# Kernel optimization log

Hardware: AMD Instinct MI355X
Metric: run time of the kernel (lower is better)

## Reference

```python
import jax, jax.numpy as jnp
import numpy as np

B, S, D = 8, 1024, 1024
H, DH = 16, 64
FF = 4096
EPS = 1e-5


def setup_inputs() -> dict:
    key = jax.random.key(0)
    ks = jax.random.split(key, 16)
    sd = 1.0 / np.sqrt(D)
    sp = 1.0 / np.sqrt(H * DH)
    sf = 1.0 / np.sqrt(FF)
    return {
        "x": jax.random.normal(ks[0], (B, S, D), jnp.float32),
        # per-head QKV projections stacked: [H, D, DH]
        "wq": jax.random.uniform(ks[1], (H, D, DH), jnp.float32, -sd, sd),
        "bq": jax.random.uniform(ks[2], (H, DH), jnp.float32, -sd, sd),
        "wk": jax.random.uniform(ks[3], (H, D, DH), jnp.float32, -sd, sd),
        "bk": jax.random.uniform(ks[4], (H, DH), jnp.float32, -sd, sd),
        "wv": jax.random.uniform(ks[5], (H, D, DH), jnp.float32, -sd, sd),
        "bv": jax.random.uniform(ks[6], (H, DH), jnp.float32, -sd, sd),
        "wo": jax.random.uniform(ks[7], (H * DH, D), jnp.float32, -sp, sp),
        "bo": jax.random.uniform(ks[8], (D,), jnp.float32, -sp, sp),
        "w1": jax.random.uniform(ks[9], (D, FF), jnp.float32, -sd, sd),
        "b1": jax.random.uniform(ks[10], (FF,), jnp.float32, -sd, sd),
        "w2": jax.random.uniform(ks[11], (FF, D), jnp.float32, -sf, sf),
        "b2": jax.random.uniform(ks[12], (D,), jnp.float32, -sf, sf),
        "g1": jnp.ones((D,), jnp.float32),
        "be1": jnp.zeros((D,), jnp.float32),
        "g2": jnp.ones((D,), jnp.float32),
        "be2": jnp.zeros((D,), jnp.float32),
    }


def _layernorm(x, g, b):
    mu = jnp.mean(x, axis=-1, keepdims=True)
    var = jnp.mean((x - mu) ** 2, axis=-1, keepdims=True)
    return (x - mu) * jax.lax.rsqrt(var + EPS) * g + b


def reference(x, wq, bq, wk, bk, wv, bv, wo, bo, w1, b1, w2, b2, g1, be1, g2, be2):
    # batched multi-head attention (math identical to the per-head torch loop)
    q = jnp.einsum('bsd,hde->bhse', x, wq) + bq[None, :, None, :]
    k = jnp.einsum('bsd,hde->bhse', x, wk) + bk[None, :, None, :]
    v = jnp.einsum('bsd,hde->bhse', x, wv) + bv[None, :, None, :]
    scores = jnp.einsum('bhse,bhte->bhst', q, k) / jnp.sqrt(jnp.float32(DH))
    probs = jax.nn.softmax(scores, axis=-1)
    ctx = jnp.einsum('bhst,bhte->bhse', probs, v)  # [B,H,S,DH]
    ctx = ctx.transpose(0, 2, 1, 3).reshape(B, S, H * DH)  # concat over heads
    attn = ctx @ wo + bo
    # dropout is identity in eval mode
    x = _layernorm(x + attn, g1, be1)
    ffn = jax.nn.relu(x @ w1 + b1) @ w2 + b2
    x = _layernorm(x + ffn, g2, be2)
    return x
```

## Files before the change

### kernel.cpp

```cpp
#include <hip/hip_runtime.h>
#include <hip/hip_bf16.h>

#define Bb 8
#define Ss 1024
#define Dd 1024
#define Hh 16
#define DHh 64
#define FFf 4096

typedef __hip_bfloat16 bf16;
typedef __attribute__((ext_vector_type(8))) __bf16 bf16x8;
typedef __attribute__((ext_vector_type(4))) float f32x4;

__device__ __forceinline__ unsigned short f2bu(float f) {
  __hip_bfloat16 h = __float2bfloat16(f);
  return __builtin_bit_cast(unsigned short, h);
}

#define MFMA16(a, b, c) __builtin_amdgcn_mfma_f32_16x16x32_bf16((a), (b), (c), 0, 0, 0)

__device__ __forceinline__ void gl_lds16(const void* g, void* l) {
  __builtin_amdgcn_global_load_lds(
      (const __attribute__((address_space(1))) unsigned int*)g,
      (__attribute__((address_space(3))) unsigned int*)l, 16, 0, 0);
}

__global__ __launch_bounds__(256) void f32_to_bf16_vec(const float* __restrict__ in,
                                                       bf16* __restrict__ out, int n4) {
  int i = blockIdx.x * 256 + threadIdx.x;
  if (i < n4) {
    float4 v = ((const float4*)in)[i];
    union { unsigned short u[4]; uint2 q; } r;
    r.u[0] = f2bu(v.x); r.u[1] = f2bu(v.y); r.u[2] = f2bu(v.z); r.u[3] = f2bu(v.w);
    ((uint2*)out)[i] = r.q;
  }
}

__global__ __launch_bounds__(256) void transpose_f32_bf16(const float* __restrict__ src,
                                                          bf16* __restrict__ dst,
                                                          int R, int C,
                                                          long sbatch, long dbatch) {
  __shared__ float tile[32][33];
  src += (size_t)blockIdx.z * sbatch;
  dst += (size_t)blockIdx.z * dbatch;
  int c0 = blockIdx.x * 32, r0 = blockIdx.y * 32;
  int tx = threadIdx.x & 31;
  int ty = threadIdx.x >> 5;
#pragma unroll
  for (int kk = 0; kk < 4; ++kk)
    tile[ty + kk * 8][tx] = src[(size_t)(r0 + ty + kk * 8) * C + c0 + tx];
  __syncthreads();
#pragma unroll
  for (int kk = 0; kk < 4; ++kk)
    dst[(size_t)(c0 + ty + kk * 8) * R + r0 + tx] = __float2bfloat16(tile[tx][ty + kk * 8]);
}

enum { EPI_QKV = 0, EPI_WO = 1, EPI_FFN1 = 2, EPI_FFN2 = 3 };

template <int EPI>
__global__ __launch_bounds__(256) void gemm_bt(const bf16* __restrict__ A,
                                               const bf16* __restrict__ Bt,
                                               int M, int N, int K,
                                               const float* __restrict__ bias0,
                                               const float* __restrict__ bias1,
                                               const float* __restrict__ bias2,
                                               void* __restrict__ o0,
                                               void* __restrict__ o1,
                                               void* __restrict__ o2) {
  __shared__ __align__(16) unsigned char sm[16384];
  const int t = threadIdx.x;
  const int lane = t & 63;
  const int w = t >> 6;
  const int wr = w >> 1;
  const int wc = w & 1;
  const int m0 = blockIdx.x * 128;
  const int n0 = blockIdx.y * 128;

  f32x4 acc[4][4];
  const f32x4 z4 = {0.f, 0.f, 0.f, 0.f};
#pragma unroll
  for (int i = 0; i < 4; ++i)
#pragma unroll
    for (int j = 0; j < 4; ++j) acc[i][j] = z4;

  const int srow = lane >> 2;
  const int sseg = lane & 3;
  const int ks = lane >> 4;
  const int rl = lane & 15;

  for (int kt = 0; kt < K; kt += 32) {
    __syncthreads();
#pragma unroll
    for (int r = 0; r < 2; ++r) {
      const int arow = r * 64 + w * 16 + srow;
      const int aseg = sseg ^ (arow & 3);
      gl_lds16(A + ((size_t)(m0 + arow) * K + kt + aseg * 8),
               sm + r * 4096 + w * 1024);
      const int brow = r * 64 + w * 16 + srow;
      const int bseg = sseg ^ (brow & 3);
      gl_lds16(Bt + ((size_t)(n0 + brow) * K + kt + bseg * 8),
               sm + 8192 + r * 4096 + w * 1024);
    }
    __syncthreads();
    bf16x8 a[4], b[4];
#pragma unroll
    for (int i = 0; i < 4; ++i) {
      const int row = wr * 64 + i * 16 + rl;
      a[i] = *(const bf16x8*)(sm + row * 64 + (ks ^ (row & 3)) * 16);
      const int col = wc * 64 + i * 16 + rl;
      b[i] = *(const bf16x8*)(sm + 8192 + col * 64 + (ks ^ (col & 3)) * 16);
    }
#pragma unroll
    for (int i = 0; i < 4; ++i)
#pragma unroll
      for (int j = 0; j < 4; ++j) acc[i][j] = MFMA16(a[i], b[j], acc[i][j]);
  }

  const int rbase = (lane >> 4) * 4;
  if constexpr (EPI == EPI_QKV) {
    const int which = n0 >> 10;
    const float* bias = which == 0 ? bias0 : (which == 1 ? bias1 : bias2);
    bf16* dst = (bf16*)(which == 0 ? o0 : (which == 1 ? o1 : o2));
#pragma unroll
    for (int i = 0; i < 4; ++i) {
#pragma unroll
      for (int j = 0; j < 4; ++j) {
        const int gcol = n0 + wc * 64 + j * 16 + rl;
        const int cc = gcol & 1023;
        const int hh = cc >> 6, e = cc & 63;
        const float bval = bias[cc];
#pragma unroll
        for (int p = 0; p < 4; ++p) {
          const int grow = m0 + wr * 64 + i * 16 + rbase + p;
          const int bidx = grow >> 10, s = grow & 1023;
          if (which == 2) {
            dst[(((size_t)bidx * Hh + hh) * DHh + e) * Ss + s] =
                __float2bfloat16(acc[i][j][p] + bval);
          } else {
            dst[(((size_t)bidx * Hh + hh) * Ss + s) * DHh + e] =
                __float2bfloat16(acc[i][j][p] + bval);
          }
        }
      }
    }
  } else if constexpr (EPI == EPI_WO || EPI == EPI_FFN2) {
    float* dst = (float*)o0;
#pragma unroll
    for (int i = 0; i < 4; ++i) {
#pragma unroll
      for (int j = 0; j < 4; ++j) {
        const int gcol = n0 + wc * 64 + j * 16 + rl;
        const float bval = bias0[gcol];
#pragma unroll
        for (int p = 0; p < 4; ++p) {
          const int grow = m0 + wr * 64 + i * 16 + rbase + p;
          dst[(size_t)grow * N + gcol] = acc[i][j][p] + bval;
        }
      }
    }
  } else {
    bf16* dst = (bf16*)o0;
#pragma unroll
    for (int i = 0; i < 4; ++i) {
#pragma unroll
      for (int j = 0; j < 4; ++j) {
        const int gcol = n0 + wc * 64 + j * 16 + rl;
        const float bval = bias0[gcol];
#pragma unroll
        for (int p = 0; p < 4; ++p) {
          const int grow = m0 + wr * 64 + i * 16 + rbase + p;
          dst[(size_t)grow * N + gcol] =
              __float2bfloat16(fmaxf(acc[i][j][p] + bval, 0.f));
        }
      }
    }
  }
}

__global__ __launch_bounds__(256) void attn_kernel(const bf16* __restrict__ q,
                                                   const bf16* __restrict__ k,
                                                   const bf16* __restrict__ v,
                                                   bf16* __restrict__ ctx) {
  __shared__ __align__(16) unsigned short Kl[64 * 64];
  __shared__ __align__(16) unsigned short Vt[64 * 64];
  __shared__ __align__(16) unsigned short Pl[4 * 16 * 72];

  const int bid = blockIdx.x;
  const int xcd = bid & 7;
  const int s8 = bid >> 3;
  const int hg = xcd + 8 * (s8 >> 4);
  const int qi = s8 & 15;
  const int b = hg >> 4, h = hg & 15;
  const int q0 = qi * 64;
  const size_t head = (size_t)hg << 16;
  const bf16* Qp = q + head;
  const bf16* Kp = k + head;
  const bf16* Vp = v + head;

  const int t = threadIdx.x;
  const int w = t >> 6;
  const int lane = t & 63;
  const int rl = lane & 15;
  const int ks = lane >> 4;
  const int rx = rl & 7;

  const int qrow = q0 + w * 16 + rl;
  const bf16x8 aq0 = *(const bf16x8*)(Qp + (size_t)qrow * 64 + ks * 8);
  const bf16x8 aq1 = *(const bf16x8*)(Qp + (size_t)qrow * 64 + 32 + ks * 8);

  f32x4 o[4];
  const f32x4 z4 = {0.f, 0.f, 0.f, 0.f};
#pragma unroll
  for (int c = 0; c < 4; ++c) o[c] = z4;
  float m4[4] = {-1e30f, -1e30f, -1e30f, -1e30f};
  float l4[4] = {0.f, 0.f, 0.f, 0.f};

  const int srow8 = lane >> 3;
  const int sseg = lane & 7;
  unsigned short* Pw = Pl + w * 16 * 72;
  const float scale = 0.125f;

  for (int kv0 = 0; kv0 < Ss; kv0 += 64) {
    __syncthreads();
#pragma unroll
    for (int r = 0; r < 2; ++r) {
      const int rb = w * 16 + r * 8;
      const int row = rb + srow8;
      gl_lds16(Kp + (size_t)(kv0 + row) * 64 + (sseg ^ (row & 7)) * 8,
               Kl + rb * 64);
      gl_lds16(Vp + (size_t)row * Ss + kv0 + (sseg ^ (row & 7)) * 8,
               Vt + rb * 64);
    }
    __syncthreads();

    f32x4 s4[4];
#pragma unroll
    for (int f = 0; f < 4; ++f) s4[f] = z4;
#pragma unroll
    for (int f = 0; f < 4; ++f) {
      const int row = f * 16 + rl;
      const bf16x8 b0 = *(const bf16x8*)(Kl + row * 64 + (ks ^ rx) * 8);
      const bf16x8 b1 = *(const bf16x8*)(Kl + row * 64 + ((4 + ks) ^ rx) * 8);
      s4[f] = MFMA16(aq0, b0, s4[f]);
      s4[f] = MFMA16(aq1, b1, s4[f]);
    }

    float mx[4], sm[4];
#pragma unroll
    for (int j = 0; j < 4; ++j) {
      s4[0][j] *= scale; s4[1][j] *= scale; s4[2][j] *= scale; s4[3][j] *= scale;
      mx[j] = fmaxf(fmaxf(s4[0][j], s4[1][j]), fmaxf(s4[2][j], s4[3][j]));
    }
#pragma unroll
    for (int mm = 1; mm < 16; mm <<= 1)
#pragma unroll
      for (int j = 0; j < 4; ++j) mx[j] = fmaxf(mx[j], __shfl_xor(mx[j], mm, 64));
#pragma unroll
    for (int j = 0; j < 4; ++j) {
      const float mn = fmaxf(m4[j], mx[j]);
      const float corr = __expf(m4[j] - mn);
      m4[j] = mn;
#pragma unroll
      for (int f = 0; f < 4; ++f) s4[f][j] = __expf(s4[f][j] - mn);
      sm[j] = (s4[0][j] + s4[1][j]) + (s4[2][j] + s4[3][j]);
      l4[j] *= corr;
#pragma unroll
      for (int c = 0; c < 4; ++c) o[c][j] *= corr;
    }
#pragma unroll
    for (int mm = 1; mm < 16; mm <<= 1)
#pragma unroll
      for (int j = 0; j < 4; ++j) sm[j] += __shfl_xor(sm[j], mm, 64);
#pragma unroll
    for (int j = 0; j < 4; ++j) l4[j] += sm[j];

#pragma unroll
    for (int f = 0; f < 4; ++f)
#pragma unroll
      for (int j = 0; j < 4; ++j)
        Pw[(ks * 4 + j) * 72 + f * 16 + rl] = f2bu(s4[f][j]);
    asm volatile("s_waitcnt lgkmcnt(0)" ::: "memory");
    __builtin_amdgcn_sched_barrier(0);
    const bf16x8 pa0 = *(const bf16x8*)(Pw + rl * 72 + ks * 8);
    const bf16x8 pa1 = *(const bf16x8*)(Pw + rl * 72 + 32 + ks * 8);

#pragma unroll
    for (int c = 0; c < 4; ++c) {
      const int row = c * 16 + rl;
      const bf16x8 v0 = *(const bf16x8*)(Vt + row * 64 + (ks ^ rx) * 8);
      const bf16x8 v1 = *(const bf16x8*)(Vt + row * 64 + ((4 + ks) ^ rx) * 8);
      o[c] = MFMA16(pa0, v0, o[c]);
      o[c] = MFMA16(pa1, v1, o[c]);
    }
  }

  float inv[4];
#pragma unroll
  for (int j = 0; j < 4; ++j) inv[j] = 1.0f / l4[j];
#pragma unroll
  for (int c = 0; c < 4; ++c) {
#pragma unroll
    for (int j = 0; j < 4; ++j) {
      const int sq = q0 + w * 16 + ks * 4 + j;
      const int dh = c * 16 + rl;
      ctx[(((size_t)b * Ss + sq) * Hh + h) * DHh + dh] =
          __float2bfloat16(o[c][j] * inv[j]);
    }
  }
}

__global__ __launch_bounds__(256) void ln_fused(const float* __restrict__ a,
                                                const float* __restrict__ bsrc,
                                                const float* __restrict__ g,
                                                const float* __restrict__ be,
                                                float* __restrict__ of,
                                                bf16* __restrict__ ob) {
  const int row = blockIdx.x, t = threadIdx.x;
  const float4 va = ((const float4*)(a + (size_t)row * Dd))[t];
  const float4 vb = ((const float4*)(bsrc + (size_t)row * Dd))[t];
  const float x0 = va.x + vb.x, x1 = va.y + vb.y, x2 = va.z + vb.z, x3 = va.w + vb.w;
  float s = x0 + x1 + x2 + x3;
  float qq = x0 * x0 + x1 * x1 + x2 * x2 + x3 * x3;
#pragma unroll
  for (int m = 1; m < 64; m <<= 1) {
    s += __shfl_xor(s, m, 64);
    qq += __shfl_xor(qq, m, 64);
  }
  __shared__ float ss[4], sq2[4];
  if ((t & 63) == 0) {
    ss[t >> 6] = s;
    sq2[t >> 6] = qq;
  }
  __syncthreads();
  s = ss[0] + ss[1] + ss[2] + ss[3];
  qq = sq2[0] + sq2[1] + sq2[2] + sq2[3];
  const float mu = s * (1.0f / Dd);
  const float var = qq * (1.0f / Dd) - mu * mu;
  const float rs = rsqrtf(var + 1e-5f);
  const float4 gv = ((const float4*)g)[t];
  const float4 bv = ((const float4*)be)[t];
  const float y0 = (x0 - mu) * rs * gv.x + bv.x;
  const float y1 = (x1 - mu) * rs * gv.y + bv.y;
  const float y2 = (x2 - mu) * rs * gv.z + bv.z;
  const float y3 = (x3 - mu) * rs * gv.w + bv.w;
  if (of) ((float4*)(of + (size_t)row * Dd))[t] = make_float4(y0, y1, y2, y3);
  if (ob) {
    union { unsigned short u[4]; uint2 qv; } r;
    r.u[0] = f2bu(y0); r.u[1] = f2bu(y1); r.u[2] = f2bu(y2); r.u[3] = f2bu(y3);
    ((uint2*)(ob + (size_t)row * Dd))[t] = r.qv;
  }
}

extern "C" void kernel_launch(void* const* d_in, const int* in_sizes, int n_in,
                              void* d_out, int out_size, void* d_ws, size_t ws_size,
                              hipStream_t stream) {
  const float* x   = (const float*)d_in[0];
  const float* wq  = (const float*)d_in[1];
  const float* bq  = (const float*)d_in[2];
  const float* wk  = (const float*)d_in[3];
  const float* bk  = (const float*)d_in[4];
  const float* wv  = (const float*)d_in[5];
  const float* bv  = (const float*)d_in[6];
  const float* wo  = (const float*)d_in[7];
  const float* bo  = (const float*)d_in[8];
  const float* w1  = (const float*)d_in[9];
  const float* b1  = (const float*)d_in[10];
  const float* w2  = (const float*)d_in[11];
  const float* b2  = (const float*)d_in[12];
  const float* g1  = (const float*)d_in[13];
  const float* be1 = (const float*)d_in[14];
  const float* g2  = (const float*)d_in[15];
  const float* be2 = (const float*)d_in[16];
  float* out = (float*)d_out;

  char* ws = (char*)d_ws;
  const size_t MB = 1u << 20;
  bf16* qb    = (bf16*)(ws + 0);
  bf16* kb    = (bf16*)(ws + 16 * MB);
  bf16* vvb   = (bf16*)(ws + 32 * MB);
  bf16* xb    = (bf16*)(ws + 48 * MB);
  bf16* hb    = (bf16*)(ws + 0);
  bf16* ctx   = (bf16*)(ws + 64 * MB);
  float* y    = (float*)(ws + 80 * MB);
  float* x1f  = (float*)(ws + 112 * MB);
  bf16* x1b   = (bf16*)(ws + 144 * MB);
  bf16* btqkv = (bf16*)(ws + 160 * MB);
  bf16* wot   = (bf16*)(ws + 166 * MB);
  bf16* w1t   = (bf16*)(ws + 168 * MB);
  bf16* w2t   = (bf16*)(ws + 176 * MB);

  f32_to_bf16_vec<<<8192, 256, 0, stream>>>(x, xb, Bb * Ss * Dd / 4);
  transpose_f32_bf16<<<dim3(2, 32, 16), 256, 0, stream>>>(wq, btqkv + 0 * 1048576,
                                                          Dd, DHh, 65536, 65536);
  transpose_f32_bf16<<<dim3(2, 32, 16), 256, 0, stream>>>(wk, btqkv + 1 * 1048576,
                                                          Dd, DHh, 65536, 65536);
  transpose_f32_bf16<<<dim3(2, 32, 16), 256, 0, stream>>>(wv, btqkv + 2 * 1048576,
                                                          Dd, DHh, 65536, 65536);
  transpose_f32_bf16<<<dim3(32, 32, 1), 256, 0, stream>>>(wo, wot, Hh * DHh, Dd, 0, 0);
  transpose_f32_bf16<<<dim3(128, 32, 1), 256, 0, stream>>>(w1, w1t, Dd, FFf, 0, 0);
  transpose_f32_bf16<<<dim3(32, 128, 1), 256, 0, stream>>>(w2, w2t, FFf, Dd, 0, 0);

  gemm_bt<EPI_QKV><<<dim3(64, 24), 256, 0, stream>>>(
      xb, btqkv, Bb * Ss, 3 * Hh * DHh, Dd, bq, bk, bv, qb, kb, vvb);

  attn_kernel<<<2048, 256, 0, stream>>>(qb, kb, vvb, ctx);

  gemm_bt<EPI_WO><<<dim3(64, 8), 256, 0, stream>>>(
      ctx, wot, Bb * Ss, Dd, Hh * DHh, bo, nullptr, nullptr, y, nullptr, nullptr);

  ln_fused<<<Bb * Ss, 256, 0, stream>>>(x, y, g1, be1, x1f, x1b);

  gemm_bt<EPI_FFN1><<<dim3(64, 32), 256, 0, stream>>>(
      x1b, w1t, Bb * Ss, FFf, Dd, b1, nullptr, nullptr, hb, nullptr, nullptr);
  gemm_bt<EPI_FFN2><<<dim3(64, 8), 256, 0, stream>>>(
      hb, w2t, Bb * Ss, Dd, FFf, b2, nullptr, nullptr, y, nullptr, nullptr);

  ln_fused<<<Bb * Ss, 256, 0, stream>>>(x1f, y, g2, be2, out, nullptr);
}
```

Measured before the change: 596.4 us.

## Replace 128x128 GEMM with double-buffered 256x256 tiled GEMM using staged prefetch

Replaces the 128x128-tile, K=32 single-buffered GEMM with a 256x256-tile, K=64 kernel using 512 threads, 128KB of dynamic LDS and double buffering. Loads for the next A tile and the tile after next for B are issued in between MFMA quarter-steps, with barriers, setprio and manual vmcnt waits, so global loads overlap compute. An XCD-aware block swizzle is added. The larger tiles reduce global traffic per FLOP but lower the block count: WO and FFN2 run only 128 blocks on a 256-CU device, which risks under-occupancy. The 128KB LDS request also limits residency per CU.

```diff
diff --git a/kernel.cpp b/kernel.cpp
--- a/kernel.cpp
+++ b/kernel.cpp
@@ -57,88 +57,163 @@
 
 enum { EPI_QKV = 0, EPI_WO = 1, EPI_FFN1 = 2, EPI_FFN2 = 3 };
 
+__device__ __forceinline__ void stage_tile(const bf16* __restrict__ G, int ldK,
+                                           int row0, int t, int u,
+                                           unsigned char* ldsbase, int tid) {
+  const int r = u * 64 + (tid >> 3);
+  const int seg = (tid & 7) ^ (((tid >> 3) & 1) << 2);
+  gl_lds16(G + (size_t)(row0 + r) * ldK + t * 64 + seg * 8,
+           ldsbase + u * 8192 + (tid >> 6) * 1024);
+}
+
 template <int EPI>
-__global__ __launch_bounds__(256) void gemm_bt(const bf16* __restrict__ A,
-                                               const bf16* __restrict__ Bt,
-                                               int M, int N, int K,
-                                               const float* __restrict__ bias0,
-                                               const float* __restrict__ bias1,
-                                               const float* __restrict__ bias2,
-                                               void* __restrict__ o0,
-                                               void* __restrict__ o1,
-                                               void* __restrict__ o2) {
-  __shared__ __align__(16) unsigned char sm[16384];
-  const int t = threadIdx.x;
-  const int lane = t & 63;
-  const int w = t >> 6;
-  const int wr = w >> 1;
-  const int wc = w & 1;
-  const int m0 = blockIdx.x * 128;
-  const int n0 = blockIdx.y * 128;
-
-  f32x4 acc[4][4];
+__global__ __launch_bounds__(512, 2) void gemm256(const bf16* __restrict__ A,
+                                                  const bf16* __restrict__ Bt,
+                                                  int M, int N, int K,
+                                                  const float* __restrict__ bias0,
+                                                  const float* __restrict__ bias1,
+                                                  const float* __restrict__ bias2,
+                                                  void* __restrict__ o0,
+                                                  void* __restrict__ o1,
+                                                  void* __restrict__ o2) {
+  extern __shared__ __align__(16) unsigned char sm[];
+  const int tid = threadIdx.x;
+  const int lane = tid & 63;
+  const int w = tid >> 6;
+  const int wr = w >> 2, wc = w & 3;
+  const int rl = lane & 15, ks4 = lane >> 4;
+  const int NTm = M >> 8, NTn = N >> 8;
+  const int nwg = NTm * NTn;
+  const int swz = (blockIdx.x & 7) * (nwg >> 3) + (blockIdx.x >> 3);
+  const int mt = swz % NTm, nt = swz / NTm;
+  const int m0 = mt << 8, n0 = nt << 8;
+  const int NT = K >> 6;
+
+  f32x4 acc[8][4];
   const f32x4 z4 = {0.f, 0.f, 0.f, 0.f};
 #pragma unroll
-  for (int i = 0; i < 4; ++i)
+  for (int i = 0; i < 8; ++i)
 #pragma unroll
     for (int j = 0; j < 4; ++j) acc[i][j] = z4;
 
-  const int srow = lane >> 2;
-  const int sseg = lane & 3;
-  const int ks = lane >> 4;
-  const int rl = lane & 15;
-
-  for (int kt = 0; kt < K; kt += 32) {
-    __syncthreads();
-#pragma unroll
-    for (int r = 0; r < 2; ++r) {
-      const int arow = r * 64 + w * 16 + srow;
-      const int aseg = sseg ^ (arow & 3);
-      gl_lds16(A + ((size_t)(m0 + arow) * K + kt + aseg * 8),
-               sm + r * 4096 + w * 1024);
-      const int brow = r * 64 + w * 16 + srow;
-      const int bseg = sseg ^ (brow & 3);
-      gl_lds16(Bt + ((size_t)(n0 + brow) * K + kt + bseg * 8),
-               sm + 8192 + r * 4096 + w * 1024);
-    }
-    __syncthreads();
-    bf16x8 a[4], b[4];
-#pragma unroll
-    for (int i = 0; i < 4; ++i) {
-      const int row = wr * 64 + i * 16 + rl;
-      a[i] = *(const bf16x8*)(sm + row * 64 + (ks ^ (row & 3)) * 16);
-      const int col = wc * 64 + i * 16 + rl;
-      b[i] = *(const bf16x8*)(sm + 8192 + col * 64 + (ks ^ (col & 3)) * 16);
-    }
-#pragma unroll
-    for (int i = 0; i < 4; ++i)
-#pragma unroll
-      for (int j = 0; j < 4; ++j) acc[i][j] = MFMA16(a[i], b[j], acc[i][j]);
-  }
-
-  const int rbase = (lane >> 4) * 4;
+#pragma unroll
+  for (int u = 0; u < 4; ++u) stage_tile(A, K, m0, 0, u, sm, tid);
+#pragma unroll
+  for (int u = 0; u < 4; ++u) stage_tile(Bt, K, n0, 0, u, sm + 32768, tid);
+  if (NT > 1) {
+#pragma unroll
+    for (int u = 0; u < 4; ++u) stage_tile(Bt, K, n0, 1, u, sm + 65536 + 32768, tid);
+    asm volatile("s_waitcnt vmcnt(4)" ::: "memory");
+  } else {
+    asm volatile("s_waitcnt vmcnt(0)" ::: "memory");
+  }
+  __builtin_amdgcn_s_barrier();
+
+  for (int t = 0; t < NT; ++t) {
+    unsigned char* Al = sm + ((t & 1) << 16);
+    unsigned char* Bl = Al + 32768;
+    unsigned char* AlN = sm + (((t + 1) & 1) << 16);
+    bf16x8 bfr[4][2], afr[2][2];
+
+#pragma unroll
+    for (int fc = 0; fc < 4; ++fc)
+#pragma unroll
+      for (int kk = 0; kk < 2; ++kk) {
+        const int rr = wc * 64 + fc * 16 + rl;
+        bfr[fc][kk] = *(const bf16x8*)(Bl + rr * 128 + ((kk ^ (rr & 1)) << 6) + ks4 * 16);
+      }
+#pragma unroll
+    for (int i = 0; i < 2; ++i)
+#pragma unroll
+      for (int kk = 0; kk < 2; ++kk) {
+        const int r = wr * 128 + i * 16 + rl;
+        afr[i][kk] = *(const bf16x8*)(Al + r * 128 + ((kk ^ (r & 1)) << 6) + ks4 * 16);
+      }
+    if (t + 1 < NT) {
+      stage_tile(A, K, m0, t + 1, 0, AlN, tid);
+      stage_tile(A, K, m0, t + 1, 2, AlN, tid);
+    }
+    __builtin_amdgcn_s_barrier();
+    __builtin_amdgcn_s_setprio(1);
+#pragma unroll
+    for (int i = 0; i < 2; ++i)
+#pragma unroll
+      for (int fc = 0; fc < 4; ++fc)
+#pragma unroll
+        for (int kk = 0; kk < 2; ++kk)
+          acc[i][fc] = MFMA16(afr[i][kk], bfr[fc][kk], acc[i][fc]);
+    __builtin_amdgcn_s_setprio(0);
+    __builtin_amdgcn_s_barrier();
+
+#pragma unroll
+    for (int q = 1; q < 4; ++q) {
+#pragma unroll
+      for (int i = 0; i < 2; ++i)
+#pragma unroll
+        for (int kk = 0; kk < 2; ++kk) {
+          const int r = wr * 128 + (q * 2 + i) * 16 + rl;
+          afr[i][kk] = *(const bf16x8*)(Al + r * 128 + ((kk ^ (r & 1)) << 6) + ks4 * 16);
+        }
+      if (q == 1) {
+        if (t + 1 < NT) {
+          stage_tile(A, K, m0, t + 1, 1, AlN, tid);
+          stage_tile(A, K, m0, t + 1, 3, AlN, tid);
+        }
+      } else if (q == 2) {
+        if (t + 2 < NT) {
+          stage_tile(Bt, K, n0, t + 2, 0, Bl, tid);
+          stage_tile(Bt, K, n0, t + 2, 1, Bl, tid);
+        }
+      } else {
+        if (t + 2 < NT) {
+          stage_tile(Bt, K, n0, t + 2, 2, Bl, tid);
+          stage_tile(Bt, K, n0, t + 2, 3, Bl, tid);
+        }
+      }
+      __builtin_amdgcn_s_barrier();
+      __builtin_amdgcn_s_setprio(1);
+#pragma unroll
+      for (int i = 0; i < 2; ++i)
+#pragma unroll
+        for (int fc = 0; fc < 4; ++fc)
+#pragma unroll
+          for (int kk = 0; kk < 2; ++kk)
+            acc[q * 2 + i][fc] = MFMA16(afr[i][kk], bfr[fc][kk], acc[q * 2 + i][fc]);
+      __builtin_amdgcn_s_setprio(0);
+      if (q == 3) {
+        if (t + 2 < NT) {
+          asm volatile("s_waitcnt vmcnt(4)" ::: "memory");
+        } else if (t + 1 < NT) {
+          asm volatile("s_waitcnt vmcnt(0)" ::: "memory");
+        }
+      }
+      __builtin_amdgcn_s_barrier();
+    }
+  }
+
+  const int rbase = ks4 * 4;
   if constexpr (EPI == EPI_QKV) {
     const int which = n0 >> 10;
     const float* bias = which == 0 ? bias0 : (which == 1 ? bias1 : bias2);
     bf16* dst = (bf16*)(which == 0 ? o0 : (which == 1 ? o1 : o2));
 #pragma unroll
-    for (int i = 0; i < 4; ++i) {
-#pragma unroll
-      for (int j = 0; j < 4; ++j) {
-        const int gcol = n0 + wc * 64 + j * 16 + rl;
+    for (int fr = 0; fr < 8; ++fr) {
+#pragma unroll
+      for (int fc = 0; fc < 4; ++fc) {
+        const int gcol = n0 + wc * 64 + fc * 16 + rl;
         const int cc = gcol & 1023;
         const int hh = cc >> 6, e = cc & 63;
         const float bval = bias[cc];
 #pragma unroll
         for (int p = 0; p < 4; ++p) {
-          const int grow = m0 + wr * 64 + i * 16 + rbase + p;
+          const int grow = m0 + wr * 128 + fr * 16 + rbase + p;
           const int bidx = grow >> 10, s = grow & 1023;
           if (which == 2) {
             dst[(((size_t)bidx * Hh + hh) * DHh + e) * Ss + s] =
-                __float2bfloat16(acc[i][j][p] + bval);
+                __float2bfloat16(acc[fr][fc][p] + bval);
           } else {
             dst[(((size_t)bidx * Hh + hh) * Ss + s) * DHh + e] =
-                __float2bfloat16(acc[i][j][p] + bval);
+                __float2bfloat16(acc[fr][fc][p] + bval);
           }
         }
       }
@@ -146,31 +221,31 @@
   } else if constexpr (EPI == EPI_WO || EPI == EPI_FFN2) {
     float* dst = (float*)o0;
 #pragma unroll
-    for (int i = 0; i < 4; ++i) {
-#pragma unroll
-      for (int j = 0; j < 4; ++j) {
-        const int gcol = n0 + wc * 64 + j * 16 + rl;
+    for (int fr = 0; fr < 8; ++fr) {
+#pragma unroll
+      for (int fc = 0; fc < 4; ++fc) {
+        const int gcol = n0 + wc * 64 + fc * 16 + rl;
         const float bval = bias0[gcol];
 #pragma unroll
         for (int p = 0; p < 4; ++p) {
-          const int grow = m0 + wr * 64 + i * 16 + rbase + p;
-          dst[(size_t)grow * N + gcol] = acc[i][j][p] + bval;
+          const int grow = m0 + wr * 128 + fr * 16 + rbase + p;
+          dst[(size_t)grow * N + gcol] = acc[fr][fc][p] + bval;
         }
       }
     }
   } else {
     bf16* dst = (bf16*)o0;
 #pragma unroll
-    for (int i = 0; i < 4; ++i) {
-#pragma unroll
-      for (int j = 0; j < 4; ++j) {
-        const int gcol = n0 + wc * 64 + j * 16 + rl;
+    for (int fr = 0; fr < 8; ++fr) {
+#pragma unroll
+      for (int fc = 0; fc < 4; ++fc) {
+        const int gcol = n0 + wc * 64 + fc * 16 + rl;
         const float bval = bias0[gcol];
 #pragma unroll
         for (int p = 0; p < 4; ++p) {
-          const int grow = m0 + wr * 64 + i * 16 + rbase + p;
+          const int grow = m0 + wr * 128 + fr * 16 + rbase + p;
           dst[(size_t)grow * N + gcol] =
-              __float2bfloat16(fmaxf(acc[i][j][p] + bval, 0.f));
+              __float2bfloat16(fmaxf(acc[fr][fc][p] + bval, 0.f));
         }
       }
     }
@@ -400,19 +475,19 @@
   transpose_f32_bf16<<<dim3(128, 32, 1), 256, 0, stream>>>(w1, w1t, Dd, FFf, 0, 0);
   transpose_f32_bf16<<<dim3(32, 128, 1), 256, 0, stream>>>(w2, w2t, FFf, Dd, 0, 0);
 
-  gemm_bt<EPI_QKV><<<dim3(64, 24), 256, 0, stream>>>(
+  gemm256<EPI_QKV><<<384, 512, 131072, stream>>>(
       xb, btqkv, Bb * Ss, 3 * Hh * DHh, Dd, bq, bk, bv, qb, kb, vvb);
 
   attn_kernel<<<2048, 256, 0, stream>>>(qb, kb, vvb, ctx);
 
-  gemm_bt<EPI_WO><<<dim3(64, 8), 256, 0, stream>>>(
+  gemm256<EPI_WO><<<128, 512, 131072, stream>>>(
       ctx, wot, Bb * Ss, Dd, Hh * DHh, bo, nullptr, nullptr, y, nullptr, nullptr);
 
   ln_fused<<<Bb * Ss, 256, 0, stream>>>(x, y, g1, be1, x1f, x1b);
 
-  gemm_bt<EPI_FFN1><<<dim3(64, 32), 256, 0, stream>>>(
+  gemm256<EPI_FFN1><<<512, 512, 131072, stream>>>(
       x1b, w1t, Bb * Ss, FFf, Dd, b1, nullptr, nullptr, hb, nullptr, nullptr);
-  gemm_bt<EPI_FFN2><<<dim3(64, 8), 256, 0, stream>>>(
+  gemm256<EPI_FFN2><<<128, 512, 131072, stream>>>(
       hb, w2t, Bb * Ss, Dd, FFf, b2, nullptr, nullptr, y, nullptr, nullptr);
 
   ln_fused<<<Bb * Ss, 256, 0, stream>>>(x1f, y, g2, be2, out, nullptr);
```

Result: slower. 700.3 us (+17.4%).

## Double GEMM k-tile depth and register-prefetch next K/V tile in attention

Applied to the files above, without the earlier changes.

The GEMM kernel now stages 64-wide K tiles (32 KB LDS) with an 8-way XOR swizzle, doing two MFMAs per fragment pair per barrier pair. This halves the number of sync rounds per output tile. The attention kernel replaces direct global-to-LDS loads with register prefetch of the next K/V tile, issued after the current tile is written to LDS, so the global loads overlap with compute. The cost is higher LDS use, which may lower occupancy, and extra VGPRs for the prefetch registers.

```diff
diff --git a/kernel.cpp b/kernel.cpp
--- a/kernel.cpp
+++ b/kernel.cpp
@@ -57,6 +57,15 @@
 
 enum { EPI_QKV = 0, EPI_WO = 1, EPI_FFN1 = 2, EPI_FFN2 = 3 };
 
+__device__ __forceinline__ void stage_u(const bf16* __restrict__ G, int ldK,
+                                        int row0, int kt, int u,
+                                        unsigned char* ldsbase, int tid) {
+  const int r = u * 32 + (tid >> 3);
+  const int seg = (tid & 7) ^ (r & 7);
+  gl_lds16(G + (size_t)(row0 + r) * ldK + kt + seg * 8,
+           ldsbase + u * 4096 + (tid >> 6) * 1024);
+}
+
 template <int EPI>
 __global__ __launch_bounds__(256) void gemm_bt(const bf16* __restrict__ A,
                                                const bf16* __restrict__ Bt,
@@ -67,7 +76,7 @@
                                                void* __restrict__ o0,
                                                void* __restrict__ o1,
                                                void* __restrict__ o2) {
-  __shared__ __align__(16) unsigned char sm[16384];
+  __shared__ __align__(16) unsigned char sm[32768];
   const int t = threadIdx.x;
   const int lane = t & 63;
   const int w = t >> 6;
@@ -75,6 +84,7 @@
   const int wc = w & 1;
   const int m0 = blockIdx.x * 128;
   const int n0 = blockIdx.y * 128;
+  const int rl = lane & 15, ks = lane >> 4;
 
   f32x4 acc[4][4];
   const f32x4 z4 = {0.f, 0.f, 0.f, 0.f};
@@ -83,40 +93,35 @@
 #pragma unroll
     for (int j = 0; j < 4; ++j) acc[i][j] = z4;
 
-  const int srow = lane >> 2;
-  const int sseg = lane & 3;
-  const int ks = lane >> 4;
-  const int rl = lane & 15;
-
-  for (int kt = 0; kt < K; kt += 32) {
+  for (int kt = 0; kt < K; kt += 64) {
     __syncthreads();
 #pragma unroll
-    for (int r = 0; r < 2; ++r) {
-      const int arow = r * 64 + w * 16 + srow;
-      const int aseg = sseg ^ (arow & 3);
-      gl_lds16(A + ((size_t)(m0 + arow) * K + kt + aseg * 8),
-               sm + r * 4096 + w * 1024);
-      const int brow = r * 64 + w * 16 + srow;
-      const int bseg = sseg ^ (brow & 3);
-      gl_lds16(Bt + ((size_t)(n0 + brow) * K + kt + bseg * 8),
-               sm + 8192 + r * 4096 + w * 1024);
-    }
+    for (int u = 0; u < 4; ++u) stage_u(A, K, m0, kt, u, sm, t);
+#pragma unroll
+    for (int u = 0; u < 4; ++u) stage_u(Bt, K, n0, kt, u, sm + 16384, t);
     __syncthreads();
-    bf16x8 a[4], b[4];
+
+    bf16x8 a[4][2], b[4][2];
 #pragma unroll
     for (int i = 0; i < 4; ++i) {
-      const int row = wr * 64 + i * 16 + rl;
-      a[i] = *(const bf16x8*)(sm + row * 64 + (ks ^ (row & 3)) * 16);
-      const int col = wc * 64 + i * 16 + rl;
-      b[i] = *(const bf16x8*)(sm + 8192 + col * 64 + (ks ^ (col & 3)) * 16);
+#pragma unroll
+      for (int kk = 0; kk < 2; ++kk) {
+        const int row = wr * 64 + i * 16 + rl;
+        a[i][kk] = *(const bf16x8*)(sm + row * 128 + (((kk * 4 + ks) ^ (row & 7)) << 4));
+        const int col = wc * 64 + i * 16 + rl;
+        b[i][kk] = *(const bf16x8*)(sm + 16384 + col * 128 + (((kk * 4 + ks) ^ (col & 7)) << 4));
+      }
     }
 #pragma unroll
     for (int i = 0; i < 4; ++i)
 #pragma unroll
-      for (int j = 0; j < 4; ++j) acc[i][j] = MFMA16(a[i], b[j], acc[i][j]);
-  }
-
-  const int rbase = (lane >> 4) * 4;
+      for (int j = 0; j < 4; ++j)
+#pragma unroll
+        for (int kk = 0; kk < 2; ++kk)
+          acc[i][j] = MFMA16(a[i][kk], b[j][kk], acc[i][j]);
+  }
+
+  const int rbase = ks * 4;
   if constexpr (EPI == EPI_QKV) {
     const int which = n0 >> 10;
     const float* bias = which == 0 ? bias0 : (which == 1 ? bias1 : bias2);
@@ -215,21 +220,29 @@
   float m4[4] = {-1e30f, -1e30f, -1e30f, -1e30f};
   float l4[4] = {0.f, 0.f, 0.f, 0.f};
 
-  const int srow8 = lane >> 3;
-  const int sseg = lane & 7;
+  const int rt = t >> 2;
+  const int st = t & 3;
+  const int wof0 = rt * 64 + ((st ^ (rt & 7)) << 3);
+  const int wof1 = rt * 64 + (((st + 4) ^ (rt & 7)) << 3);
   unsigned short* Pw = Pl + w * 16 * 72;
   const float scale = 0.125f;
 
+  bf16x8 kr0 = *(const bf16x8*)(Kp + (size_t)rt * 64 + st * 8);
+  bf16x8 kr1 = *(const bf16x8*)(Kp + (size_t)rt * 64 + (st + 4) * 8);
+  bf16x8 vr0 = *(const bf16x8*)(Vp + (size_t)rt * Ss + st * 8);
+  bf16x8 vr1 = *(const bf16x8*)(Vp + (size_t)rt * Ss + (st + 4) * 8);
+
   for (int kv0 = 0; kv0 < Ss; kv0 += 64) {
     __syncthreads();
-#pragma unroll
-    for (int r = 0; r < 2; ++r) {
-      const int rb = w * 16 + r * 8;
-      const int row = rb + srow8;
-      gl_lds16(Kp + (size_t)(kv0 + row) * 64 + (sseg ^ (row & 7)) * 8,
-               Kl + rb * 64);
-      gl_lds16(Vp + (size_t)row * Ss + kv0 + (sseg ^ (row & 7)) * 8,
-               Vt + rb * 64);
+    *(bf16x8*)(Kl + wof0) = kr0;
+    *(bf16x8*)(Kl + wof1) = kr1;
+    *(bf16x8*)(Vt + wof0) = vr0;
+    *(bf16x8*)(Vt + wof1) = vr1;
+    if (kv0 + 64 < Ss) {
+      kr0 = *(const bf16x8*)(Kp + (size_t)(kv0 + 64 + rt) * 64 + st * 8);
+      kr1 = *(const bf16x8*)(Kp + (size_t)(kv0 + 64 + rt) * 64 + (st + 4) * 8);
+      vr0 = *(const bf16x8*)(Vp + (size_t)rt * Ss + kv0 + 64 + st * 8);
+      vr1 = *(const bf16x8*)(Vp + (size_t)rt * Ss + kv0 + 64 + (st + 4) * 8);
     }
     __syncthreads();
 
```

Result: faster. 560.8 us (-6.0%).
